# Kernel optimization log

Measured on AMD Instinct MI355X. Metric: run time of the kernel, lower is better.

Reference implementation:

```python
import jax, jax.numpy as jnp
import numpy as np


def _ramp_filter(H):
    # skimage-style Fourier ramp filter: 2*|f| with f = fftfreq(H)
    f = np.fft.fftfreq(H)
    return (2.0 * np.abs(f)).astype(np.float32)


def setup_inputs() -> dict:
    key = jax.random.key(0)
    N, H_in, W_in, D_out = 8, 768, 360, 512
    radon_image = jax.random.normal(key, (N, 1, H_in, W_in), dtype=jnp.float32)
    hG = jnp.asarray(_ramp_filter(H_in)).reshape(1, 1, H_in, 1)
    return {"radon_image": radon_image, "hG": hG, "D_out": D_out}


def reference(radon_image, hG, D_out):
    N, _, H, W = radon_image.shape
    D = D_out
    # --- Fourier-domain ramp filtering (2D FFT, multiply by real filter along detector axis, real ifft) ---
    X = jnp.fft.fft2(radon_image[:, 0])                     # [N, H, W] complex
    h = hG[0, 0, :, 0]                                      # [H]
    filt = jnp.real(jnp.fft.ifft2(X * h[None, :, None])).astype(radon_image.dtype)  # [N, H, W]

    # --- backprojection grids (matches np.mgrid / tG construction) ---
    Xg, Yg = jnp.meshgrid(jnp.arange(D), jnp.arange(D), indexing="ij")
    xpr = (Xg - D // 2).astype(jnp.float32)
    ypr = (Yg - D // 2).astype(jnp.float32)
    th = (jnp.pi / 180.0) * jnp.linspace(0.0, 180.0, W, endpoint=False)  # [W]
    txs = -1.0 + jnp.arange(W, dtype=jnp.float32) * (2.0 / (W - 1))     # [W]

    hH = H // 2
    sy = (H - 1) / 2.0   # align_corners=True y scale
    sx = (W - 1) / 2.0   # align_corners=True x scale

    def body(recon, angle):
        th_i, tx_i = angle
        t = ypr * jnp.cos(th_i) - xpr * jnp.sin(th_i)       # [D, D]
        py = (t / hH + 1.0) * sy                            # pixel y coords [D, D]
        px = (tx_i + 1.0) * sx                              # scalar pixel x coord
        x0 = jnp.floor(px).astype(jnp.int32)
        wx = px - x0
        y0 = jnp.floor(py).astype(jnp.int32)
        wy = py - y0

        def samp_col(xi):
            vx = ((xi >= 0) & (xi < W)).astype(filt.dtype)
            col = filt[:, :, jnp.clip(xi, 0, W - 1)]        # [N, H]

            def samp_y(yi):
                vy = ((yi >= 0) & (yi < H)).astype(filt.dtype)
                return col[:, jnp.clip(yi, 0, H - 1)] * vy  # [N, D, D] zero-padded

            v = samp_y(y0) * (1.0 - wy) + samp_y(y0 + 1) * wy
            return v * vx

        val = samp_col(x0) * (1.0 - wx) + samp_col(x0 + 1) * wx  # [N, D, D]
        return recon + val, None

    recon0 = jnp.zeros((N, D, D), dtype=radon_image.dtype)
    recon, _ = jax.lax.scan(body, recon0, (th, txs))
    return (recon * (jnp.pi / (2.0 * W)))[:, None]          # [N, 1, D, D]
```

## Files before the change

### kernel.cpp

```cpp
#include <hip/hip_runtime.h>
#include <math.h>

#define N_IMG 8
#define H 768
#define W 360
#define D 512
#define SY 383.5f
#define SC 0.00436332312998582394f
#define NC 24
#define IPAD 384

typedef __fp16 h2 __attribute__((ext_vector_type(2)));
struct H2X2 { h2 a, b; };
typedef short short8 __attribute__((ext_vector_type(8)));
typedef float f32x4 __attribute__((ext_vector_type(4)));

__device__ inline unsigned bf16pair(float a, float b) {
    unsigned ua = __builtin_bit_cast(unsigned, a);
    unsigned ub = __builtin_bit_cast(unsigned, b);
    ua += 0x7FFFu + ((ua >> 16) & 1u);
    ub += 0x7FFFu + ((ub >> 16) & 1u);
    return (ua >> 16) | (ub & 0xFFFF0000u);
}

__global__ void build_g_kernel(const float* __restrict__ hG, float* __restrict__ g) {
    int m = blockIdx.x;
    int lane = threadIdx.x;
    float s = 0.f;
#pragma unroll
    for (int q = 0; q < 12; ++q) {
        int k = lane + 64 * q;
        int prod = (k * m) % H;
        float angr = (float)prod * 0.00818123086872313911f;
        s += hG[k] * cosf(angr);
    }
#pragma unroll
    for (int off = 32; off > 0; off >>= 1) s += __shfl_down(s, off);
    if (lane == 0) g[m] = s * (1.0f / (float)H);
}

#define KSTEPS 10

__global__ void build_angbg_kernel(const float* __restrict__ g, uint4* __restrict__ Bg,
                                   float2* __restrict__ ang) {
    int b = blockIdx.x;
    int t = threadIdx.x;
    if (b < 40) {
        int idx = b * 64 + t;
        int L  = idx & 63;
        int tj = idx >> 6;
        int nn = (tj & 3) * 16 + (L & 15);
        int kb = (tj >> 2) * 32 + (L >> 4) * 8;
        float bf[8];
#pragma unroll
        for (int s = 0; s < 8; ++s) {
            int d = nn + 128 - (kb + s);
            d += (d < 0) ? H : 0;
            bf[s] = g[d];
        }
        Bg[idx] = (uint4){bf16pair(bf[0], bf[1]), bf16pair(bf[2], bf[3]),
                          bf16pair(bf[4], bf[5]), bf16pair(bf[6], bf[7])};
    } else {
#pragma unroll
        for (int q = 0; q < 6; ++q) {
            int i = t + 64 * q;
            if (i < W) {
                float th = (float)i * 0.00872664625997164788f;
                float r = SY / 384.0f;
                ang[i] = make_float2(cosf(th) * r, -sinf(th) * r);
            }
        }
    }
}

__global__ __launch_bounds__(256)
void build_rc_kernel(const float* __restrict__ radon, uint4* __restrict__ rcC,
                     float4* __restrict__ out4) {
    __shared__ float xs[32][65];

    const int i0 = blockIdx.x * 64;
    const int c  = blockIdx.y;
    const int n  = blockIdx.z;
    const int tid = threadIdx.x;

    {
        int flat = ((n * NC) + c) * 6 + blockIdx.x;
        if (flat < 1024) {
            out4[flat * 512 + tid]       = make_float4(0.f, 0.f, 0.f, 0.f);
            out4[flat * 512 + 256 + tid] = make_float4(0.f, 0.f, 0.f, 0.f);
        }
    }

    {
        int mr    = tid >> 3;
        int lane8 = tid & 7;
        int ib = i0 + lane8 * 8;
        const float* src = radon + ((size_t)n * H + 32 * c + mr) * W + ib;
        float4 v0, v1;
        if (ib + 7 < W) {
            v0 = *(const float4*)src;
            v1 = *(const float4*)(src + 4);
        } else {
            v0 = make_float4(0.f, 0.f, 0.f, 0.f);
            v1 = make_float4(0.f, 0.f, 0.f, 0.f);
        }
        *(float4*)&xs[mr][lane8 * 8]     = v0;
        *(float4*)&xs[mr][lane8 * 8 + 4] = v1;
    }
    __syncthreads();

    const int il  = tid >> 2;
    const int oct = tid & 3;
    float v[8];
#pragma unroll
    for (int s = 0; s < 8; ++s) v[s] = xs[oct * 8 + s][il];
    uint4 pk = {bf16pair(v[0], v[1]), bf16pair(v[2], v[3]),
                bf16pair(v[4], v[5]), bf16pair(v[6], v[7])};
    rcC[(((size_t)n * NC + c) * IPAD + i0 + il) * 4 + oct] = pk;
}

__global__ __launch_bounds__(256)
void filt_gemm_kernel(const uint4* __restrict__ rcC, const uint4* __restrict__ Bg,
                      unsigned short* __restrict__ colp) {
    __shared__ _Float16 lx[16][64][4];

    const int grp = blockIdx.z;
    const int i0 = blockIdx.y * 16;
    const int y0 = blockIdx.x * 64;
    const int wv = threadIdx.x >> 6;
    const int L  = threadIdx.x & 63;

    const int c0 = (y0 / 32 + 20) % NC;
    const uint4* An = rcC + (size_t)(grp * 4 + wv) * NC * IPAD * 4;
    const int arow = i0 + (L & 15);
    const int aoff = L >> 4;

    f32x4 acc[4];
#pragma unroll
    for (int j = 0; j < 4; ++j) acc[j] = (f32x4){0.f, 0.f, 0.f, 0.f};

    for (int t = 0; t < KSTEPS; ++t) {
        int c = c0 + t;
        c -= (c >= NC) ? NC : 0;
        short8 a = __builtin_bit_cast(short8, An[((size_t)c * IPAD + arow) * 4 + aoff]);
#pragma unroll
        for (int j = 0; j < 4; ++j) {
            short8 b = __builtin_bit_cast(short8, Bg[(t * 4 + j) * 64 + L]);
            acc[j] = __builtin_amdgcn_mfma_f32_16x16x32_bf16(a, b, acc[j], 0, 0, 0);
        }
    }

#pragma unroll
    for (int j = 0; j < 4; ++j) {
#pragma unroll
        for (int r = 0; r < 4; ++r) {
            int ilc = (L >> 4) * 4 + r;
            int ylc = j * 16 + (L & 15);
            lx[ilc][ylc][wv] = (_Float16)(acc[j][r] * SC);
        }
    }
    __syncthreads();

    unsigned short* cp = colp + (size_t)grp * W * H * 4;
#pragma unroll
    for (int k = 0; k < 4; ++k) {
        int e = threadIdx.x + k * 256;
        int ilc = e >> 6, ylc = e & 63;
        int ig = i0 + ilc;
        if (ig < W) {
            uint2 v = *(const uint2*)&lx[ilc][ylc][0];
            *(uint2*)&cp[((size_t)ig * H + y0 + ylc) * 4] = v;
        }
    }
}

__global__ __launch_bounds__(512, 8)
void backproj_kernel(const unsigned short* __restrict__ colp,
                     const float2* __restrict__ angv, float* __restrict__ outb) {
    __shared__ __align__(16) H2X2 colh[2][H];

    const int bid = blockIdx.x;
    const int bz  = bid & 7;
    const int tle = bid >> 3;
    const int g  = bz >> 2;
    const int aq = bz & 3;
    const int a0 = aq * (W / 4);
    const int u0 = (tle >> 3) * 32;
    const int v0 = (tle & 7) * 64;
    const int tid = threadIdx.x;
    const int lane = tid & 63;
    const int tu = tid >> 6;

    const float vf = (float)(v0 + lane - D / 2);
    float uf[4];
#pragma unroll
    for (int r = 0; r < 4; ++r) uf[r] = (float)(u0 + tu + 8 * r - D / 2);

    const h2 hz = {(__fp16)0.f, (__fp16)0.f};
    float acc[4][4];
    h2 haccA[4], haccB[4];
#pragma unroll
    for (int r = 0; r < 4; ++r) {
#pragma unroll
        for (int nn = 0; nn < 4; ++nn) acc[r][nn] = 0.f;
        haccA[r] = hz;
        haccB[r] = hz;
    }

    const uint2* cp = (const uint2*)colp + (size_t)g * W * H;

    const int y1 = tid;
    const int y2 = tid + 512;

    {
        const int ab = a0 * H;
        colh[0][y1] = __builtin_bit_cast(H2X2, cp[ab + y1]);
        if (tid < 256) colh[0][y2] = __builtin_bit_cast(H2X2, cp[ab + y2]);
    }
    __syncthreads();

    for (int j = 0; j < W / 4; ++j) {
        int a = a0 + j;
        int an = (j + 1 < W / 4) ? (a + 1) : a;
        const int ab = an * H;
        uint2 d = cp[ab + y1];
        uint2 e = make_uint2(0u, 0u);
        if (tid < 256) e = cp[ab + y2];

        const int cb2 = j & 1;
        float2 AB = angv[a];
        float base = fmaf(vf, AB.x, SY);
#pragma unroll
        for (int r = 0; r < 4; ++r) {
            float py = fmaf(uf[r], AB.y, base);
            float wy = __builtin_amdgcn_fractf(py);
            int iy = (int)py;
            uint2 lo_raw = *(const uint2*)&colh[cb2][iy];
            uint2 hi_raw = *(const uint2*)&colh[cb2][iy + 1];
            H2X2 lo = __builtin_bit_cast(H2X2, lo_raw);
            H2X2 hi = __builtin_bit_cast(H2X2, hi_raw);
            h2 wy2 = __builtin_amdgcn_cvt_pkrtz(wy, wy);
            haccA[r] += lo.a + wy2 * (hi.a - lo.a);
            haccB[r] += lo.b + wy2 * (hi.b - lo.b);
        }

        if ((j & 15) == 15) {
#pragma unroll
            for (int r = 0; r < 4; ++r) {
                acc[r][0] += (float)haccA[r].x;
                acc[r][1] += (float)haccA[r].y;
                acc[r][2] += (float)haccB[r].x;
                acc[r][3] += (float)haccB[r].y;
                haccA[r] = hz;
                haccB[r] = hz;
            }
        }

        colh[cb2 ^ 1][y1] = __builtin_bit_cast(H2X2, d);
        if (tid < 256) colh[cb2 ^ 1][y2] = __builtin_bit_cast(H2X2, e);
        __syncthreads();
    }

#pragma unroll
    for (int r = 0; r < 4; ++r) {
        acc[r][0] += (float)haccA[r].x;
        acc[r][1] += (float)haccA[r].y;
        acc[r][2] += (float)haccB[r].x;
        acc[r][3] += (float)haccB[r].y;
        int u = u0 + tu + 8 * r;
#pragma unroll
        for (int nn = 0; nn < 4; ++nn) {
            size_t idx = ((size_t)(g * 4 + nn) * D + u) * D + v0 + lane;
            atomicAdd(&outb[idx], acc[r][nn]);
        }
    }
}

extern "C" void kernel_launch(void* const* d_in, const int* in_sizes, int n_in,
                              void* d_out, int out_size, void* d_ws, size_t ws_size,
                              hipStream_t stream) {
    const float* radon = (const float*)d_in[0];
    const float* hG    = (const float*)d_in[1];
    float* out = (float*)d_out;

    float*  g    = (float*)d_ws;
    float2* ang  = (float2*)((char*)d_ws + 4096);
    uint4*  Bg   = (uint4*)((char*)d_ws + 8192);
    unsigned short* colp = (unsigned short*)((char*)d_ws + 65536);
    uint4*  rcC  = (uint4*)((char*)d_ws + 4489216);

    build_g_kernel<<<H, 64, 0, stream>>>(hG, g);
    build_angbg_kernel<<<41, 64, 0, stream>>>(g, Bg, ang);
    build_rc_kernel<<<dim3(6, NC, N_IMG), 256, 0, stream>>>(radon, rcC, (float4*)out);
    filt_gemm_kernel<<<dim3(H / 64, 23, 2), 256, 0, stream>>>(rcC, Bg, colp);
    backproj_kernel<<<1024, 512, 0, stream>>>(colp, ang, out);
}
```

Baseline: 168.5 us.

## Fuse filter-kernel setup into one launch, shrink GEMM tiles, compute angles in backprojection

```diff
diff --git a/kernel.cpp b/kernel.cpp
--- a/kernel.cpp
+++ b/kernel.cpp
@@ -9,6 +9,7 @@
 #define SC 0.00436332312998582394f
 #define NC 24
 #define IPAD 384
+#define KSTEPS 10
 
 typedef __fp16 h2 __attribute__((ext_vector_type(2)));
 struct H2X2 { h2 a, b; };
@@ -23,53 +24,42 @@
     return (ua >> 16) | (ub & 0xFFFF0000u);
 }
 
-__global__ void build_g_kernel(const float* __restrict__ hG, float* __restrict__ g) {
-    int m = blockIdx.x;
-    int lane = threadIdx.x;
-    float s = 0.f;
-#pragma unroll
-    for (int q = 0; q < 12; ++q) {
-        int k = lane + 64 * q;
-        int prod = (k * m) % H;
-        float angr = (float)prod * 0.00818123086872313911f;
-        s += hG[k] * cosf(angr);
-    }
-#pragma unroll
-    for (int off = 32; off > 0; off >>= 1) s += __shfl_down(s, off);
-    if (lane == 0) g[m] = s * (1.0f / (float)H);
-}
-
-#define KSTEPS 10
-
-__global__ void build_angbg_kernel(const float* __restrict__ g, uint4* __restrict__ Bg,
-                                   float2* __restrict__ ang) {
-    int b = blockIdx.x;
-    int t = threadIdx.x;
-    if (b < 40) {
-        int idx = b * 64 + t;
-        int L  = idx & 63;
-        int tj = idx >> 6;
-        int nn = (tj & 3) * 16 + (L & 15);
-        int kb = (tj >> 2) * 32 + (L >> 4) * 8;
+__global__ __launch_bounds__(256)
+void build_bg_kernel(const float* __restrict__ hG, uint4* __restrict__ Bg) {
+    __shared__ float hGs[H];
+    __shared__ float gl[96];
+
+    const int t = blockIdx.x;
+    const int tid = threadIdx.x;
+
+#pragma unroll
+    for (int q = 0; q < 3; ++q) hGs[tid + 256 * q] = hG[tid + 256 * q];
+    __syncthreads();
+
+    if (tid < 192) {
+        int l = tid >> 1, h = tid & 1;
+        int d = 97 - 32 * t + l;
+        int dm = d + ((d < 0) ? H : 0);
+        float s = 0.f;
+#pragma unroll 4
+        for (int q = 0; q < 384; ++q) {
+            int k = h * 384 + q;
+            int prod = (k * dm) % H;
+            s += hGs[k] * __builtin_amdgcn_cosf((float)prod * (1.0f / 768.0f));
+        }
+        s += __shfl_xor(s, 1);
+        if (h == 0) gl[l] = s * (1.0f / (float)H);
+    }
+    __syncthreads();
+
+    {
+        int j = tid >> 6, L = tid & 63;
+        int base = 16 * j + (L & 15) + 31 - (L >> 4) * 8;
         float bf[8];
 #pragma unroll
-        for (int s = 0; s < 8; ++s) {
-            int d = nn + 128 - (kb + s);
-            d += (d < 0) ? H : 0;
-            bf[s] = g[d];
-        }
-        Bg[idx] = (uint4){bf16pair(bf[0], bf[1]), bf16pair(bf[2], bf[3]),
-                          bf16pair(bf[4], bf[5]), bf16pair(bf[6], bf[7])};
-    } else {
-#pragma unroll
-        for (int q = 0; q < 6; ++q) {
-            int i = t + 64 * q;
-            if (i < W) {
-                float th = (float)i * 0.00872664625997164788f;
-                float r = SY / 384.0f;
-                ang[i] = make_float2(cosf(th) * r, -sinf(th) * r);
-            }
-        }
+        for (int s = 0; s < 8; ++s) bf[s] = gl[base - s];
+        Bg[(t * 4 + j) * 64 + L] = (uint4){bf16pair(bf[0], bf[1]), bf16pair(bf[2], bf[3]),
+                                           bf16pair(bf[4], bf[5]), bf16pair(bf[6], bf[7])};
     }
 }
 
@@ -122,11 +112,11 @@
 __global__ __launch_bounds__(256)
 void filt_gemm_kernel(const uint4* __restrict__ rcC, const uint4* __restrict__ Bg,
                       unsigned short* __restrict__ colp) {
-    __shared__ _Float16 lx[16][64][4];
+    __shared__ _Float16 lx[16][32][4];
 
     const int grp = blockIdx.z;
     const int i0 = blockIdx.y * 16;
-    const int y0 = blockIdx.x * 64;
+    const int y0 = blockIdx.x * 32;
     const int wv = threadIdx.x >> 6;
     const int L  = threadIdx.x & 63;
 
@@ -135,23 +125,23 @@
     const int arow = i0 + (L & 15);
     const int aoff = L >> 4;
 
-    f32x4 acc[4];
-#pragma unroll
-    for (int j = 0; j < 4; ++j) acc[j] = (f32x4){0.f, 0.f, 0.f, 0.f};
+    f32x4 acc[2];
+    acc[0] = (f32x4){0.f, 0.f, 0.f, 0.f};
+    acc[1] = (f32x4){0.f, 0.f, 0.f, 0.f};
 
     for (int t = 0; t < KSTEPS; ++t) {
         int c = c0 + t;
         c -= (c >= NC) ? NC : 0;
         short8 a = __builtin_bit_cast(short8, An[((size_t)c * IPAD + arow) * 4 + aoff]);
 #pragma unroll
-        for (int j = 0; j < 4; ++j) {
+        for (int j = 0; j < 2; ++j) {
             short8 b = __builtin_bit_cast(short8, Bg[(t * 4 + j) * 64 + L]);
             acc[j] = __builtin_amdgcn_mfma_f32_16x16x32_bf16(a, b, acc[j], 0, 0, 0);
         }
     }
 
 #pragma unroll
-    for (int j = 0; j < 4; ++j) {
+    for (int j = 0; j < 2; ++j) {
 #pragma unroll
         for (int r = 0; r < 4; ++r) {
             int ilc = (L >> 4) * 4 + r;
@@ -163,9 +153,9 @@
 
     unsigned short* cp = colp + (size_t)grp * W * H * 4;
 #pragma unroll
-    for (int k = 0; k < 4; ++k) {
-        int e = threadIdx.x + k * 256;
-        int ilc = e >> 6, ylc = e & 63;
+    for (int k2 = 0; k2 < 2; ++k2) {
+        int e = threadIdx.x + k2 * 256;
+        int ilc = e >> 5, ylc = e & 31;
         int ig = i0 + ilc;
         if (ig < W) {
             uint2 v = *(const uint2*)&lx[ilc][ylc][0];
@@ -175,9 +165,9 @@
 }
 
 __global__ __launch_bounds__(512, 8)
-void backproj_kernel(const unsigned short* __restrict__ colp,
-                     const float2* __restrict__ angv, float* __restrict__ outb) {
+void backproj_kernel(const unsigned short* __restrict__ colp, float* __restrict__ outb) {
     __shared__ __align__(16) H2X2 colh[2][H];
+    __shared__ float2 angs[W / 4];
 
     const int bid = blockIdx.x;
     const int bz  = bid & 7;
@@ -212,6 +202,11 @@
     const int y1 = tid;
     const int y2 = tid + 512;
 
+    if (tid < W / 4) {
+        float th = (float)(a0 + tid) * 0.00872664625997164788f;
+        float r = SY / 384.0f;
+        angs[tid] = make_float2(cosf(th) * r, -sinf(th) * r);
+    }
     {
         const int ab = a0 * H;
         colh[0][y1] = __builtin_bit_cast(H2X2, cp[ab + y1]);
@@ -228,7 +223,7 @@
         if (tid < 256) e = cp[ab + y2];
 
         const int cb2 = j & 1;
-        float2 AB = angv[a];
+        float2 AB = angs[j];
         float base = fmaf(vf, AB.x, SY);
 #pragma unroll
         for (int r = 0; r < 4; ++r) {
@@ -283,15 +278,12 @@
     const float* hG    = (const float*)d_in[1];
     float* out = (float*)d_out;
 
-    float*  g    = (float*)d_ws;
-    float2* ang  = (float2*)((char*)d_ws + 4096);
     uint4*  Bg   = (uint4*)((char*)d_ws + 8192);
     unsigned short* colp = (unsigned short*)((char*)d_ws + 65536);
     uint4*  rcC  = (uint4*)((char*)d_ws + 4489216);
 
-    build_g_kernel<<<H, 64, 0, stream>>>(hG, g);
-    build_angbg_kernel<<<41, 64, 0, stream>>>(g, Bg, ang);
+    build_bg_kernel<<<10, 256, 0, stream>>>(hG, Bg);
     build_rc_kernel<<<dim3(6, NC, N_IMG), 256, 0, stream>>>(radon, rcC, (float4*)out);
-    filt_gemm_kernel<<<dim3(H / 64, 23, 2), 256, 0, stream>>>(rcC, Bg, colp);
-    backproj_kernel<<<1024, 512, 0, stream>>>(colp, ang, out);
-}
+    filt_gemm_kernel<<<dim3(24, 23, 2), 256, 0, stream>>>(rcC, Bg, colp);
+    backproj_kernel<<<1024, 512, 0, stream>>>(colp, out);
+}
```

Measured after the change: 177.0 us. 5.1% more time.
